# Performance work log

Measured on AMD Instinct MI355X. Metric: run time of the kernel, lower is better.

Reference implementation:

```python
import jax, jax.numpy as jnp
import numpy as np

N, E = 100000, 800000
H, C = 4, 32
HC = H * C


def setup_inputs() -> dict:
    key = jax.random.key(0)
    ks = jax.random.split(key, 32)

    def lin(k, fi, fo):
        return jax.random.normal(k, (fi, fo), jnp.float32) / np.sqrt(fi)

    inp = {
        "x": jax.random.normal(ks[0], (N, 2), jnp.float32),
        "edge_index": jax.random.randint(ks[1], (2, E), 0, N, jnp.int64),
        "edge_attr": jax.random.normal(ks[2], (E, 1), jnp.float32),
        # layer 0 (in=2)
        "Wq0": lin(ks[3], 2, HC), "bq0": jnp.zeros((HC,), jnp.float32),
        "Wk0": lin(ks[4], 2, HC), "bk0": jnp.zeros((HC,), jnp.float32),
        "Wv0": lin(ks[5], 2, HC), "bv0": jnp.zeros((HC,), jnp.float32),
        "We0": lin(ks[6], 1, HC),
        "Ws0": lin(ks[7], 2, HC), "bs0": jnp.zeros((HC,), jnp.float32),
        # layer 1 (in=HC)
        "Wq1": lin(ks[8], HC, HC), "bq1": jnp.zeros((HC,), jnp.float32),
        "Wk1": lin(ks[9], HC, HC), "bk1": jnp.zeros((HC,), jnp.float32),
        "Wv1": lin(ks[10], HC, HC), "bv1": jnp.zeros((HC,), jnp.float32),
        "We1": lin(ks[11], 1, HC),
        "Ws1": lin(ks[12], HC, HC), "bs1": jnp.zeros((HC,), jnp.float32),
        # classifier
        "Wc1": lin(ks[13], HC, 128), "bc1": jnp.zeros((128,), jnp.float32),
        "Wc2": lin(ks[14], 128, 64), "bc2": jnp.zeros((64,), jnp.float32),
        "Wc3": lin(ks[15], 64, 1), "bc3": jnp.zeros((1,), jnp.float32),
    }
    return inp


def _tconv(x, src, dst, edge_attr, Wq, bq, Wk, bk, Wv, bv, We, Ws, bs):
    # PyG TransformerConv (concat=True, root_weight=True, beta=False)
    n = x.shape[0]
    q = (x @ Wq + bq).reshape(n, H, C)
    k = (x @ Wk + bk).reshape(n, H, C)
    v = (x @ Wv + bv).reshape(n, H, C)
    e = (edge_attr @ We).reshape(-1, H, C)            # [E,H,C]
    k_j = k[src] + e
    v_j = v[src] + e
    alpha = jnp.einsum("ehc,ehc->eh", q[dst], k_j) / np.sqrt(C)  # [E,H]
    m = jax.ops.segment_max(alpha, dst, num_segments=n)          # [n,H]
    m = jnp.where(jnp.isfinite(m), m, 0.0)            # nodes with no in-edges
    ex = jnp.exp(alpha - m[dst])
    denom = jax.ops.segment_sum(ex, dst, num_segments=n)
    w = ex / (denom[dst] + 1e-16)                      # per-edge softmax weight
    out = jax.ops.segment_sum(v_j * w[:, :, None], dst, num_segments=n)
    return out.reshape(n, HC) + x @ Ws + bs


def reference(x, edge_index, edge_attr,
              Wq0, bq0, Wk0, bk0, Wv0, bv0, We0, Ws0, bs0,
              Wq1, bq1, Wk1, bk1, Wv1, bv1, We1, Ws1, bs1,
              Wc1, bc1, Wc2, bc2, Wc3, bc3):
    src, dst = edge_index[0], edge_index[1]
    h = jax.nn.relu(_tconv(x, src, dst, edge_attr, Wq0, bq0, Wk0, bk0, Wv0, bv0, We0, Ws0, bs0))
    h = jax.nn.relu(_tconv(h, src, dst, edge_attr, Wq1, bq1, Wk1, bk1, Wv1, bv1, We1, Ws1, bs1))
    # classifier (dropout inactive in eval)
    h = jax.nn.relu(h @ Wc1 + bc1)
    h = jax.nn.relu(h @ Wc2 + bc2)
    return h @ Wc3 + bc3
```

## Files before the change

kernel.cpp:

```cpp
#include <hip/hip_runtime.h>
#include <hip/hip_bf16.h>
#include <cstdio>
#include <cstdint>


typedef short s16x8 __attribute__((ext_vector_type(8)));
typedef float f32x4 __attribute__((ext_vector_type(4)));

static inline int cdiv(int a, int b) { return (a + b - 1) / b; }

#define EXP2F(x) __builtin_amdgcn_exp2f(x)
#define LOG2E 1.4426950408889634f
#define RSC 0.17677669529663687f

__device__ __forceinline__ float bflo(unsigned u) {
    union { unsigned i; float f; } x; x.i = u << 16; return x.f;
}
__device__ __forceinline__ float bfhi(unsigned u) {
    union { unsigned i; float f; } x; x.i = u & 0xffff0000u; return x.f;
}
__device__ __forceinline__ unsigned short f2b(float f) {
    __hip_bfloat16 h = __float2bfloat16(f);
    return *reinterpret_cast<unsigned short*>(&h);
}
__device__ __forceinline__ unsigned packbf(float lo, float hi) {
    return (unsigned)f2b(lo) | ((unsigned)f2b(hi) << 16);
}


__global__ __launch_bounds__(256) void hist_kernel(const int* __restrict__ dst, int E,
                                                   int* __restrict__ counts) {
    int e = blockIdx.x * 256 + threadIdx.x;
    if (e < E) atomicAdd(&counts[dst[e]], 1);
}

__global__ __launch_bounds__(256) void scan_sums(const int* __restrict__ counts, int n,
                                                 int* __restrict__ bsums) {
    __shared__ int red[256];
    int base = blockIdx.x * 2048 + threadIdx.x * 8;
    int s = 0;
#pragma unroll
    for (int j = 0; j < 8; ++j) {
        int i = base + j;
        if (i < n) s += counts[i];
    }
    red[threadIdx.x] = s;
    __syncthreads();
    for (int off = 128; off > 0; off >>= 1) {
        if (threadIdx.x < off) red[threadIdx.x] += red[threadIdx.x + off];
        __syncthreads();
    }
    if (threadIdx.x == 0) bsums[blockIdx.x] = red[0];
}

__global__ void scan_mid(int* bsums, int nb, int* offsets, int n) {
    if (blockIdx.x == 0 && threadIdx.x == 0) {
        int run = 0;
        for (int i = 0; i < nb; ++i) { int t = bsums[i]; bsums[i] = run; run += t; }
        offsets[n] = run;
    }
}

__global__ __launch_bounds__(256) void scan_out(const int* __restrict__ counts, int n,
                                                const int* __restrict__ bsums,
                                                int* __restrict__ offsets) {
    __shared__ int tsum[256];
    int base = blockIdx.x * 2048 + threadIdx.x * 8;
    int v[8];
    int s = 0;
#pragma unroll
    for (int j = 0; j < 8; ++j) {
        int i = base + j;
        v[j] = (i < n) ? counts[i] : 0;
        s += v[j];
    }
    tsum[threadIdx.x] = s;
    __syncthreads();
    for (int off = 1; off < 256; off <<= 1) {
        int x = (threadIdx.x >= (unsigned)off) ? tsum[threadIdx.x - off] : 0;
        __syncthreads();
        tsum[threadIdx.x] += x;
        __syncthreads();
    }
    int excl = tsum[threadIdx.x] - s + bsums[blockIdx.x];
#pragma unroll
    for (int j = 0; j < 8; ++j) {
        int i = base + j;
        if (i < n) { offsets[i] = excl; excl += v[j]; }
    }
}

__global__ __launch_bounds__(256) void scatter_kernel(const int* __restrict__ src,
                                                      const int* __restrict__ dst,
                                                      const float* __restrict__ ea, int E,
                                                      const int* __restrict__ offsets,
                                                      int* __restrict__ counts,
                                                      int2* __restrict__ csr) {
    int e = blockIdx.x * 256 + threadIdx.x;
    if (e >= E) return;
    int d = dst[e];
    int r = atomicSub(&counts[d], 1);
    int p = offsets[d] + r - 1;
    csr[p] = make_int2(src[e] << 9, __float_as_int(ea[e]));
}


__global__ __launch_bounds__(256) void pack_w_kernel(
    const float* __restrict__ Wq1, const float* __restrict__ Wk1,
    const float* __restrict__ Wv1, const float* __restrict__ Ws1,
    const float* __restrict__ Wc1, const float* __restrict__ Wc2,
    unsigned short* __restrict__ wpk,
    const float* __restrict__ Wq0, const float* __restrict__ bq0,
    const float* __restrict__ Wk0, const float* __restrict__ bk0,
    const float* __restrict__ We0, float* __restrict__ gcoef) {
    if (blockIdx.x == 352) {
        int t = threadIdx.x;
        if (t < 48) {
            int h = t / 12, r = t % 12, i = r >> 2, j = r & 3;
            const float* A = (i == 0) ? Wq0 : (i == 1) ? (Wq0 + 128) : bq0;
            const float* B = (j == 0) ? Wk0 : (j == 1) ? (Wk0 + 128) : (j == 2) ? We0 : bk0;
            float s = 0.f;
            for (int c = 0; c < 32; ++c) s += A[h * 32 + c] * B[h * 32 + c];
            gcoef[h * 12 + i * 4 + j] = s * (RSC * LOG2E);
        }
        return;
    }
    int idx = blockIdx.x * 256 + threadIdx.x;
    int local, COLS;
    const float* W;
    if (idx < 81920) {
        int m = idx >> 14;
        local = idx & 16383;
        COLS = 128;
        W = (m == 0) ? Wq1 : (m == 1) ? Wk1 : (m == 2) ? Wv1 : (m == 3) ? Ws1 : Wc1;
    } else {
        local = idx - 81920;
        COLS = 64;
        W = Wc2;
    }
    int CT = COLS >> 4;
    int j = local & 7, lane = (local >> 3) & 63, t = local >> 9;
    int ct = t % CT, kc = t / CT;
    int k = kc * 32 + ((lane >> 4) << 3) + j;
    int nn = (ct << 4) + (lane & 15);
    wpk[idx] = f2b(W[k * COLS + nn]);
}


__global__ __launch_bounds__(256) void agg0_kernel(
    const float* __restrict__ x, const float* __restrict__ gcoef,
    float4* __restrict__ agg4,
    const int* __restrict__ offsets, const int2* __restrict__ csr, int n_nodes) {
    int tid = blockIdx.x * 256 + threadIdx.x;
    int n = tid >> 2, h = tid & 3;
    if (n >= n_nodes) return;
    float2 xn = ((const float2*)x)[n];
    const float4* G4 = (const float4*)gcoef;
    float4 g0 = G4[h * 3 + 0], g1 = G4[h * 3 + 1], g2 = G4[h * 3 + 2];
    float c0 = fmaf(xn.y, g1.x, fmaf(xn.x, g0.x, g2.x));
    float c1 = fmaf(xn.y, g1.y, fmaf(xn.x, g0.y, g2.y));
    float c2 = fmaf(xn.y, g1.z, fmaf(xn.x, g0.z, g2.z));
    float c3 = fmaf(xn.y, g1.w, fmaf(xn.x, g0.w, g2.w));
    int beg = offsets[n], end = offsets[n + 1];
    float d = 0.f, X0 = 0.f, X1 = 0.f, EA = 0.f;
    for (int j = beg; j < end; ++j) {
        int2 ce = csr[j];
        float e = __int_as_float(ce.y);
        float2 xs = *(const float2*)((const char*)x + (((unsigned)ce.x) >> 6));
        float al = fmaf(c0, xs.x, fmaf(c1, xs.y, fmaf(c2, e, c3)));
        float w = EXP2F(fminf(al, 72.f));
        d += w;
        X0 = fmaf(w, xs.x, X0);
        X1 = fmaf(w, xs.y, X1);
        EA = fmaf(w, e, EA);
    }
    agg4[(size_t)n * 4 + h] = make_float4(X0, X1, EA, d);
}


__global__ __launch_bounds__(256) void expand0_kernel(
    const float* __restrict__ x, const float4* __restrict__ agg4,
    const float* __restrict__ Wv, const float* __restrict__ bv,
    const float* __restrict__ We, const float* __restrict__ Ws,
    const float* __restrict__ bs, uint2* __restrict__ H0, int n_nodes) {
    int gid = blockIdx.x * 256 + threadIdx.x;
    int n = gid >> 5, g = gid & 31;
    if (n >= n_nodes) return;
    int h = g >> 3;
    float4 ag = agg4[(size_t)n * 4 + h];
    float inv = 1.f / (ag.w + 1e-16f);
    float2 xn = ((const float2*)x)[n];
    float4 wv0 = ((const float4*)Wv)[g], wv1 = ((const float4*)(Wv + 128))[g];
    float4 we = ((const float4*)We)[g], bv4 = ((const float4*)bv)[g];
    float4 ws0 = ((const float4*)Ws)[g], ws1 = ((const float4*)(Ws + 128))[g];
    float4 bs4 = ((const float4*)bs)[g];
    float o0 = fmaf(wv0.x, ag.x, fmaf(wv1.x, ag.y, fmaf(we.x, ag.z, bv4.x * ag.w))) * inv
             + fmaf(xn.x, ws0.x, fmaf(xn.y, ws1.x, bs4.x));
    float o1 = fmaf(wv0.y, ag.x, fmaf(wv1.y, ag.y, fmaf(we.y, ag.z, bv4.y * ag.w))) * inv
             + fmaf(xn.x, ws0.y, fmaf(xn.y, ws1.y, bs4.y));
    float o2 = fmaf(wv0.z, ag.x, fmaf(wv1.z, ag.y, fmaf(we.z, ag.z, bv4.z * ag.w))) * inv
             + fmaf(xn.x, ws0.z, fmaf(xn.y, ws1.z, bs4.z));
    float o3 = fmaf(wv0.w, ag.x, fmaf(wv1.w, ag.y, fmaf(we.w, ag.z, bv4.w * ag.w))) * inv
             + fmaf(xn.x, ws0.w, fmaf(xn.y, ws1.w, bs4.w));
    uint2 o;
    o.x = packbf(fmaxf(o0, 0.f), fmaxf(o1, 0.f));
    o.y = packbf(fmaxf(o2, 0.f), fmaxf(o3, 0.f));
    H0[(size_t)n * 32 + g] = o;
}


__global__ __launch_bounds__(64) void agg1_kernel(
    const uint4* __restrict__ Q4, const unsigned short* __restrict__ KV,
    const float* __restrict__ We, const uint4* __restrict__ S4,
    uint4* __restrict__ Hout, const int* __restrict__ offsets,
    const int2* __restrict__ csr, int n_nodes) {
    int lane = threadIdx.x & 63;
    int h = lane & 15, g = lane >> 4;
    int n = blockIdx.x;
    if (n >= n_nodes) return;
    size_t rb = (size_t)n * 16;
    const float sc = RSC * LOG2E;
    uint4 qp = Q4[rb + h];
    float q0 = bflo(qp.x) * sc, q1 = bfhi(qp.x) * sc;
    float q2 = bflo(qp.y) * sc, q3 = bfhi(qp.y) * sc;
    float q4 = bflo(qp.z) * sc, q5 = bfhi(qp.z) * sc;
    float q6 = bflo(qp.w) * sc, q7 = bfhi(qp.w) * sc;
    float4 wea = ((const float4*)We)[2 * h], web = ((const float4*)We)[2 * h + 1];
    float qwe = fmaf(q7, web.w, fmaf(q6, web.z, fmaf(q5, web.y, fmaf(q4, web.x,
                fmaf(q3, wea.w, fmaf(q2, wea.z, fmaf(q1, wea.y, q0 * wea.x)))))));
    qwe += __shfl_xor(qwe, 1);
    qwe += __shfl_xor(qwe, 2);
    int beg = __builtin_amdgcn_readfirstlane(offsets[n]);
    int end = __builtin_amdgcn_readfirstlane(offsets[n + 1]);
    float dA = 0.f, eA = 0.f, dB = 0.f, eB = 0.f;
    float aA0 = 0.f, aA1 = 0.f, aA2 = 0.f, aA3 = 0.f;
    float aA4 = 0.f, aA5 = 0.f, aA6 = 0.f, aA7 = 0.f;
    float aB0 = 0.f, aB1 = 0.f, aB2 = 0.f, aB3 = 0.f;
    float aB4 = 0.f, aB5 = 0.f, aB6 = 0.f, aB7 = 0.f;
    int hb = h << 4;
    for (int t = beg; t < end; t += 8) {
        int jA = t + g, jB = jA + 4;
        bool vA = jA < end, vB = jB < end;
        int2 ceA = csr[vA ? jA : beg];
        int2 ceB = csr[vB ? jB : beg];
        float eaA = __int_as_float(ceA.y), eaB = __int_as_float(ceB.y);
        const char* kvA = (const char*)KV + (size_t)(unsigned)ceA.x + hb;
        const char* kvB = (const char*)KV + (size_t)(unsigned)ceB.x + hb;
        uint4 kA = *(const uint4*)kvA;
        uint4 vA4 = *(const uint4*)(kvA + 256);
        uint4 kB = *(const uint4*)kvB;
        uint4 vB4 = *(const uint4*)(kvB + 256);
        {
            float p = fmaf(q7, bfhi(kA.w), fmaf(q6, bflo(kA.w), fmaf(q5, bfhi(kA.z),
                      fmaf(q4, bflo(kA.z), fmaf(q3, bfhi(kA.y), fmaf(q2, bflo(kA.y),
                      fmaf(q1, bfhi(kA.x), q0 * bflo(kA.x))))))));
            p += __shfl_xor(p, 1);
            p += __shfl_xor(p, 2);
            float al = fminf(fmaf(eaA, qwe, p), 72.f);
            al = vA ? al : -3.0e38f;
            float w = EXP2F(al);
            dA += w;
            eA = fmaf(w, eaA, eA);
            aA0 = fmaf(w, bflo(vA4.x), aA0); aA1 = fmaf(w, bfhi(vA4.x), aA1);
            aA2 = fmaf(w, bflo(vA4.y), aA2); aA3 = fmaf(w, bfhi(vA4.y), aA3);
            aA4 = fmaf(w, bflo(vA4.z), aA4); aA5 = fmaf(w, bfhi(vA4.z), aA5);
            aA6 = fmaf(w, bflo(vA4.w), aA6); aA7 = fmaf(w, bfhi(vA4.w), aA7);
        }
        {
            float p = fmaf(q7, bfhi(kB.w), fmaf(q6, bflo(kB.w), fmaf(q5, bfhi(kB.z),
                      fmaf(q4, bflo(kB.z), fmaf(q3, bfhi(kB.y), fmaf(q2, bflo(kB.y),
                      fmaf(q1, bfhi(kB.x), q0 * bflo(kB.x))))))));
            p += __shfl_xor(p, 1);
            p += __shfl_xor(p, 2);
            float al = fminf(fmaf(eaB, qwe, p), 72.f);
            al = vB ? al : -3.0e38f;
            float w = EXP2F(al);
            dB += w;
            eB = fmaf(w, eaB, eB);
            aB0 = fmaf(w, bflo(vB4.x), aB0); aB1 = fmaf(w, bfhi(vB4.x), aB1);
            aB2 = fmaf(w, bflo(vB4.y), aB2); aB3 = fmaf(w, bfhi(vB4.y), aB3);
            aB4 = fmaf(w, bflo(vB4.z), aB4); aB5 = fmaf(w, bfhi(vB4.z), aB5);
            aB6 = fmaf(w, bflo(vB4.w), aB6); aB7 = fmaf(w, bfhi(vB4.w), aB7);
        }
    }
    float d = dA + dB, ea = eA + eB;
    float a0 = aA0 + aB0, a1 = aA1 + aB1, a2 = aA2 + aB2, a3 = aA3 + aB3;
    float a4 = aA4 + aB4, a5 = aA5 + aB5, a6 = aA6 + aB6, a7 = aA7 + aB7;
#pragma unroll
    for (int mk = 16; mk < 64; mk <<= 1) {
        d += __shfl_xor(d, mk);
        ea += __shfl_xor(ea, mk);
        a0 += __shfl_xor(a0, mk); a1 += __shfl_xor(a1, mk);
        a2 += __shfl_xor(a2, mk); a3 += __shfl_xor(a3, mk);
        a4 += __shfl_xor(a4, mk); a5 += __shfl_xor(a5, mk);
        a6 += __shfl_xor(a6, mk); a7 += __shfl_xor(a7, mk);
    }
    if (g == 0) {
        float inv = 1.f / (d + 1e-16f);
        uint4 sp = S4[rb + h];
        float o0 = fmaf(fmaf(wea.x, ea, a0), inv, bflo(sp.x));
        float o1 = fmaf(fmaf(wea.y, ea, a1), inv, bfhi(sp.x));
        float o2 = fmaf(fmaf(wea.z, ea, a2), inv, bflo(sp.y));
        float o3 = fmaf(fmaf(wea.w, ea, a3), inv, bfhi(sp.y));
        float o4 = fmaf(fmaf(web.x, ea, a4), inv, bflo(sp.z));
        float o5 = fmaf(fmaf(web.y, ea, a5), inv, bfhi(sp.z));
        float o6 = fmaf(fmaf(web.z, ea, a6), inv, bflo(sp.w));
        float o7 = fmaf(fmaf(web.w, ea, a7), inv, bfhi(sp.w));
        uint4 o;
        o.x = packbf(fmaxf(o0, 0.f), fmaxf(o1, 0.f));
        o.y = packbf(fmaxf(o2, 0.f), fmaxf(o3, 0.f));
        o.z = packbf(fmaxf(o4, 0.f), fmaxf(o5, 0.f));
        o.w = packbf(fmaxf(o6, 0.f), fmaxf(o7, 0.f));
        Hout[rb + h] = o;
    }
}


__global__ __launch_bounds__(256, 2) void gemm4_kernel(
    const unsigned short* __restrict__ Hb, int n_nodes,
    const unsigned short* __restrict__ wpk,
    const float* __restrict__ B0, unsigned short* __restrict__ O0, int ld0,
    const float* __restrict__ B1, unsigned short* __restrict__ O1, int ld1,
    const float* __restrict__ B2, unsigned short* __restrict__ O2, int ld2,
    const float* __restrict__ B3, unsigned short* __restrict__ O3, int ld3) {
    __shared__ __align__(16) unsigned short wbuf[16384];
    __shared__ __align__(16) char tbuf[128 * 272];
    int tid = threadIdx.x;
    int wid = tid >> 6, lane = tid & 63;
    int lr = lane & 15, lk = lane >> 4;
    int nblk = blockIdx.x * 128;

    s16x8 b[2][4];
#pragma unroll
    for (int nt = 0; nt < 2; ++nt) {
        int row = min(nblk + wid * 32 + nt * 16 + lr, n_nodes - 1);
        const s16x8* hp = (const s16x8*)(Hb + (size_t)row * 128);
#pragma unroll
        for (int kc = 0; kc < 4; ++kc) b[nt][kc] = hp[kc * 4 + lk];
    }
    const float* Bm[4] = {B0, B1, B2, B3};
    unsigned short* Om[4] = {O0, O1, O2, O3};
    int ldm[4] = {ld0, ld1, ld2, ld3};

#pragma unroll
    for (int i = 0; i < 8; ++i) {
        int c = i * 256 + tid;
        ((uint4*)wbuf)[c] = ((const uint4*)wpk)[c];
    }
#pragma unroll
    for (int mm = 0; mm < 4; ++mm) {
        __syncthreads();
        f32x4 acc[2][8];
#pragma unroll
        for (int nt = 0; nt < 2; ++nt)
#pragma unroll
            for (int ct = 0; ct < 8; ++ct) acc[nt][ct] = (f32x4){0.f, 0.f, 0.f, 0.f};
#pragma unroll
        for (int kc = 0; kc < 4; ++kc) {
#pragma unroll
            for (int ct = 0; ct < 8; ++ct) {
                s16x8 a = ((const s16x8*)wbuf)[(kc * 8 + ct) * 64 + lane];
                acc[0][ct] = __builtin_amdgcn_mfma_f32_16x16x32_bf16(a, b[0][kc], acc[0][ct], 0, 0, 0);
                acc[1][ct] = __builtin_amdgcn_mfma_f32_16x16x32_bf16(a, b[1][kc], acc[1][ct], 0, 0, 0);
            }
        }
        const float* Bp = Bm[mm];
#pragma unroll
        for (int ct = 0; ct < 8; ++ct) {
            float4 bb = *(const float4*)(Bp + ct * 16 + lk * 4);
#pragma unroll
            for (int nt = 0; nt < 2; ++nt) {
                int rnode = wid * 32 + nt * 16 + lr;
                uint2 o;
                o.x = packbf(acc[nt][ct][0] + bb.x, acc[nt][ct][1] + bb.y);
                o.y = packbf(acc[nt][ct][2] + bb.z, acc[nt][ct][3] + bb.w);
                *(uint2*)(tbuf + rnode * 272 + ct * 32 + lk * 8) = o;
            }
        }
        __syncthreads();
        unsigned short* Op = Om[mm];
        int ld = ldm[mm];
#pragma unroll
        for (int i = 0; i < 8; ++i) {
            int chunk = i * 256 + tid;
            int nd = chunk >> 4, c16 = chunk & 15;
            int ng = nblk + nd;
            uint4 v = *(const uint4*)(tbuf + nd * 272 + c16 * 16);
            if (ng < n_nodes) *(uint4*)(Op + (size_t)ng * ld + c16 * 8) = v;
        }
        if (mm < 3) {
            const uint4* ws = (const uint4*)(wpk + (mm + 1) * 16384);
#pragma unroll
            for (int i = 0; i < 8; ++i) {
                int c = i * 256 + tid;
                ((uint4*)wbuf)[c] = ws[c];
            }
        }
    }
}


__global__ __launch_bounds__(256, 2) void classifier_kernel(
    const unsigned short* __restrict__ H1b, int n_nodes,
    const unsigned short* __restrict__ wc1p, const float* __restrict__ bc1,
    const unsigned short* __restrict__ wc2p, const float* __restrict__ bc2,
    const float* __restrict__ Wc3, const float* __restrict__ bc3,
    float* __restrict__ out) {
    __shared__ __align__(16) unsigned short w1s[16384];
    __shared__ __align__(16) unsigned short w2s[8192];
    __shared__ __align__(16) char lds_raw[4 * 16 * 272];
    int tid = threadIdx.x;
    int wid = tid >> 6, lane = tid & 63;
    int lr = lane & 15, lk = lane >> 4;
    int nb = blockIdx.x * 64 + wid * 16;
    char* tile = lds_raw + wid * 16 * 272;

#pragma unroll
    for (int i = 0; i < 8; ++i)
        ((uint4*)w1s)[i * 256 + tid] = ((const uint4*)wc1p)[i * 256 + tid];
#pragma unroll
    for (int i = 0; i < 4; ++i)
        ((uint4*)w2s)[i * 256 + tid] = ((const uint4*)wc2p)[i * 256 + tid];

    s16x8 b[4];
    {
        int row = min(nb + lr, n_nodes - 1);
        const s16x8* hp = (const s16x8*)(H1b + (size_t)row * 128);
#pragma unroll
        for (int kc = 0; kc < 4; ++kc) b[kc] = hp[kc * 4 + lk];
    }
    __syncthreads();
    f32x4 acc[8];
#pragma unroll
    for (int ct = 0; ct < 8; ++ct) acc[ct] = (f32x4){0.f, 0.f, 0.f, 0.f};
#pragma unroll
    for (int kc = 0; kc < 4; ++kc)
#pragma unroll
        for (int ct = 0; ct < 8; ++ct) {
            s16x8 a = ((const s16x8*)w1s)[(kc * 8 + ct) * 64 + lane];
            acc[ct] = __builtin_amdgcn_mfma_f32_16x16x32_bf16(a, b[kc], acc[ct], 0, 0, 0);
        }
#pragma unroll
    for (int ct = 0; ct < 8; ++ct) {
        float4 bb = *(const float4*)(bc1 + ct * 16 + lk * 4);
        uint2 o;
        o.x = packbf(fmaxf(acc[ct][0] + bb.x, 0.f), fmaxf(acc[ct][1] + bb.y, 0.f));
        o.y = packbf(fmaxf(acc[ct][2] + bb.z, 0.f), fmaxf(acc[ct][3] + bb.w, 0.f));
        *(uint2*)(tile + lr * 272 + ct * 32 + lk * 8) = o;
    }
    __syncthreads();
    s16x8 b2[4];
#pragma unroll
    for (int kc = 0; kc < 4; ++kc)
        b2[kc] = *(const s16x8*)(tile + lr * 272 + kc * 64 + lk * 16);
    f32x4 acc2[4];
#pragma unroll
    for (int ct = 0; ct < 4; ++ct) acc2[ct] = (f32x4){0.f, 0.f, 0.f, 0.f};
#pragma unroll
    for (int kc = 0; kc < 4; ++kc)
#pragma unroll
        for (int ct = 0; ct < 4; ++ct) {
            s16x8 a = ((const s16x8*)w2s)[(kc * 4 + ct) * 64 + lane];
            acc2[ct] = __builtin_amdgcn_mfma_f32_16x16x32_bf16(a, b2[kc], acc2[ct], 0, 0, 0);
        }
    float part = 0.f;
#pragma unroll
    for (int ct = 0; ct < 4; ++ct) {
        int ch0 = ct * 16 + lk * 4;
        float4 bb = *(const float4*)(bc2 + ch0);
        float4 w3 = *(const float4*)(Wc3 + ch0);
        part += fmaxf(acc2[ct][0] + bb.x, 0.f) * w3.x;
        part += fmaxf(acc2[ct][1] + bb.y, 0.f) * w3.y;
        part += fmaxf(acc2[ct][2] + bb.z, 0.f) * w3.z;
        part += fmaxf(acc2[ct][3] + bb.w, 0.f) * w3.w;
    }
    part += __shfl_xor(part, 16);
    part += __shfl_xor(part, 32);
    if (lk == 0) {
        int node = nb + lr;
        if (node < n_nodes) out[node] = part + bc3[0];
    }
}


extern "C" void kernel_launch(void* const* d_in, const int* in_sizes, int n_in,
                              void* d_out, int out_size, void* d_ws, size_t ws_size,
                              hipStream_t stream) {
    const float* x = (const float*)d_in[0];
    const int* ei = (const int*)d_in[1];
    const float* ea = (const float*)d_in[2];
    const float *Wq0 = (const float*)d_in[3], *bq0 = (const float*)d_in[4];
    const float *Wk0 = (const float*)d_in[5], *bk0 = (const float*)d_in[6];
    const float *Wv0 = (const float*)d_in[7], *bv0 = (const float*)d_in[8];
    const float* We0 = (const float*)d_in[9];
    const float *Ws0 = (const float*)d_in[10], *bs0 = (const float*)d_in[11];
    const float *Wq1 = (const float*)d_in[12], *bq1 = (const float*)d_in[13];
    const float *Wk1 = (const float*)d_in[14], *bk1 = (const float*)d_in[15];
    const float *Wv1 = (const float*)d_in[16], *bv1 = (const float*)d_in[17];
    const float* We1 = (const float*)d_in[18];
    const float *Ws1 = (const float*)d_in[19], *bs1 = (const float*)d_in[20];
    const float *Wc1 = (const float*)d_in[21], *bc1 = (const float*)d_in[22];
    const float *Wc2 = (const float*)d_in[23], *bc2 = (const float*)d_in[24];
    const float *Wc3 = (const float*)d_in[25], *bc3 = (const float*)d_in[26];

    const int N = in_sizes[0] / 2;
    const int E = in_sizes[2];
    const int* src = ei;
    const int* dst = ei + E;

    size_t NM = (size_t)N * 128;
    float4* agg4 = (float4*)d_ws;
    float* gcoef = (float*)(agg4 + (size_t)N * 4);
    unsigned short* H0b = (unsigned short*)(gcoef + 64);
    unsigned short* Qb = H0b + NM;
    unsigned short* KV = Qb + NM;
    unsigned short* S1b = KV + 2 * NM;
    unsigned short* wpk = S1b + NM;
    int* counts = (int*)(wpk + 90112);
    int* offsets = counts + N;
    int* bsums = offsets + N + 1;
    int2* csr = (int2*)(bsums + 256);
    size_t need = (size_t)((char*)(csr + E) - (char*)d_ws);
    if (need > ws_size) {
        fprintf(stderr, "kernel_launch: ws too small (need %zu, have %zu)\n", need, ws_size);
        return;
    }

    const int NB_SCAN = cdiv(N, 2048);

    hipMemsetAsync(counts, 0, (size_t)N * 4, stream);
    hist_kernel<<<cdiv(E, 256), 256, 0, stream>>>(dst, E, counts);
    scan_sums<<<NB_SCAN, 256, 0, stream>>>(counts, N, bsums);
    scan_mid<<<1, 64, 0, stream>>>(bsums, NB_SCAN, offsets, N);
    scan_out<<<NB_SCAN, 256, 0, stream>>>(counts, N, bsums, offsets);
    scatter_kernel<<<cdiv(E, 256), 256, 0, stream>>>(src, dst, ea, E, offsets, counts, csr);
    pack_w_kernel<<<353, 256, 0, stream>>>(Wq1, Wk1, Wv1, Ws1, Wc1, Wc2, wpk,
                                           Wq0, bq0, Wk0, bk0, We0, gcoef);

    agg0_kernel<<<cdiv(N * 4, 256), 256, 0, stream>>>(
        x, gcoef, agg4, offsets, csr, N);
    expand0_kernel<<<cdiv(N * 32, 256), 256, 0, stream>>>(
        x, agg4, Wv0, bv0, We0, Ws0, bs0, (uint2*)H0b, N);

    gemm4_kernel<<<cdiv(N, 128), 256, 0, stream>>>(
        H0b, N, wpk,
        bq1, Qb, 128,
        bk1, KV, 256,
        bv1, KV + 128, 256,
        bs1, S1b, 128);
    agg1_kernel<<<N, 64, 0, stream>>>(
        (const uint4*)Qb, KV, We1, (const uint4*)S1b, (uint4*)S1b,
        offsets, csr, N);

    classifier_kernel<<<cdiv(N, 64), 256, 0, stream>>>(
        S1b, N, wpk + 65536, bc1, wpk + 81920, bc2, Wc3, bc3, (float*)d_out);
}
```

Before: 360.3 us.

## Fuse hist with weight packing, agg0 with expand0, and pack agg1 four waves per block

Merges the edge histogram and weight-packing kernels into one launch and fuses the layer-0 aggregation with its expansion through shared memory. This removes the agg4 intermediate buffer round trip and two kernel launches. agg1 now runs four nodes per 256-thread block instead of one node per 64-thread block, which cuts block scheduling overhead. The fused agg0x_kernel adds a block-wide barrier that can stall on high-degree nodes.

```diff
diff --git a/kernel.cpp b/kernel.cpp
--- a/kernel.cpp
+++ b/kernel.cpp
@@ -28,11 +28,55 @@
 }
 
 
-__global__ __launch_bounds__(256) void hist_kernel(const int* __restrict__ dst, int E,
-                                                   int* __restrict__ counts) {
-    int e = blockIdx.x * 256 + threadIdx.x;
-    if (e < E) atomicAdd(&counts[dst[e]], 1);
-}
+__global__ __launch_bounds__(256) void histpack_kernel(
+    const int* __restrict__ dst, int E, int* __restrict__ counts, int nb_hist,
+    const float* __restrict__ Wq1, const float* __restrict__ Wk1,
+    const float* __restrict__ Wv1, const float* __restrict__ Ws1,
+    const float* __restrict__ Wc1, const float* __restrict__ Wc2,
+    unsigned short* __restrict__ wpk,
+    const float* __restrict__ Wq0, const float* __restrict__ bq0,
+    const float* __restrict__ Wk0, const float* __restrict__ bk0,
+    const float* __restrict__ We0, float* __restrict__ gcoef) {
+    int bid = blockIdx.x;
+    if (bid < nb_hist) {
+        int e = bid * 256 + threadIdx.x;
+        if (e < E) atomicAdd(&counts[dst[e]], 1);
+        return;
+    }
+    int pb = bid - nb_hist;
+    if (pb == 352) {
+        int t = threadIdx.x;
+        if (t < 48) {
+            int h = t / 12, r = t % 12, i = r >> 2, j = r & 3;
+            const float* A = (i == 0) ? Wq0 : (i == 1) ? (Wq0 + 128) : bq0;
+            const float* B = (j == 0) ? Wk0 : (j == 1) ? (Wk0 + 128) : (j == 2) ? We0 : bk0;
+            float s = 0.f;
+            for (int c = 0; c < 32; ++c) s += A[h * 32 + c] * B[h * 32 + c];
+            gcoef[h * 12 + i * 4 + j] = s * (RSC * LOG2E);
+        }
+        return;
+    }
+    int idx = pb * 256 + threadIdx.x;
+    int local, COLS;
+    const float* W;
+    if (idx < 81920) {
+        int m = idx >> 14;
+        local = idx & 16383;
+        COLS = 128;
+        W = (m == 0) ? Wq1 : (m == 1) ? Wk1 : (m == 2) ? Wv1 : (m == 3) ? Ws1 : Wc1;
+    } else {
+        local = idx - 81920;
+        COLS = 64;
+        W = Wc2;
+    }
+    int CT = COLS >> 4;
+    int j = local & 7, lane = (local >> 3) & 63, t = local >> 9;
+    int ct = t % CT, kc = t / CT;
+    int k = kc * 32 + ((lane >> 4) << 3) + j;
+    int nn = (ct << 4) + (lane & 15);
+    wpk[idx] = f2b(W[k * COLS + nn]);
+}
+
 
 __global__ __launch_bounds__(256) void scan_sums(const int* __restrict__ counts, int n,
                                                  int* __restrict__ bsums) {
@@ -105,118 +149,80 @@
 }
 
 
-__global__ __launch_bounds__(256) void pack_w_kernel(
-    const float* __restrict__ Wq1, const float* __restrict__ Wk1,
-    const float* __restrict__ Wv1, const float* __restrict__ Ws1,
-    const float* __restrict__ Wc1, const float* __restrict__ Wc2,
-    unsigned short* __restrict__ wpk,
-    const float* __restrict__ Wq0, const float* __restrict__ bq0,
-    const float* __restrict__ Wk0, const float* __restrict__ bk0,
-    const float* __restrict__ We0, float* __restrict__ gcoef) {
-    if (blockIdx.x == 352) {
-        int t = threadIdx.x;
-        if (t < 48) {
-            int h = t / 12, r = t % 12, i = r >> 2, j = r & 3;
-            const float* A = (i == 0) ? Wq0 : (i == 1) ? (Wq0 + 128) : bq0;
-            const float* B = (j == 0) ? Wk0 : (j == 1) ? (Wk0 + 128) : (j == 2) ? We0 : bk0;
-            float s = 0.f;
-            for (int c = 0; c < 32; ++c) s += A[h * 32 + c] * B[h * 32 + c];
-            gcoef[h * 12 + i * 4 + j] = s * (RSC * LOG2E);
-        }
-        return;
-    }
-    int idx = blockIdx.x * 256 + threadIdx.x;
-    int local, COLS;
-    const float* W;
-    if (idx < 81920) {
-        int m = idx >> 14;
-        local = idx & 16383;
-        COLS = 128;
-        W = (m == 0) ? Wq1 : (m == 1) ? Wk1 : (m == 2) ? Wv1 : (m == 3) ? Ws1 : Wc1;
-    } else {
-        local = idx - 81920;
-        COLS = 64;
-        W = Wc2;
-    }
-    int CT = COLS >> 4;
-    int j = local & 7, lane = (local >> 3) & 63, t = local >> 9;
-    int ct = t % CT, kc = t / CT;
-    int k = kc * 32 + ((lane >> 4) << 3) + j;
-    int nn = (ct << 4) + (lane & 15);
-    wpk[idx] = f2b(W[k * COLS + nn]);
-}
-
-
-__global__ __launch_bounds__(256) void agg0_kernel(
+__global__ __launch_bounds__(256) void agg0x_kernel(
     const float* __restrict__ x, const float* __restrict__ gcoef,
-    float4* __restrict__ agg4,
-    const int* __restrict__ offsets, const int2* __restrict__ csr, int n_nodes) {
-    int tid = blockIdx.x * 256 + threadIdx.x;
-    int n = tid >> 2, h = tid & 3;
-    if (n >= n_nodes) return;
-    float2 xn = ((const float2*)x)[n];
-    const float4* G4 = (const float4*)gcoef;
-    float4 g0 = G4[h * 3 + 0], g1 = G4[h * 3 + 1], g2 = G4[h * 3 + 2];
-    float c0 = fmaf(xn.y, g1.x, fmaf(xn.x, g0.x, g2.x));
-    float c1 = fmaf(xn.y, g1.y, fmaf(xn.x, g0.y, g2.y));
-    float c2 = fmaf(xn.y, g1.z, fmaf(xn.x, g0.z, g2.z));
-    float c3 = fmaf(xn.y, g1.w, fmaf(xn.x, g0.w, g2.w));
-    int beg = offsets[n], end = offsets[n + 1];
-    float d = 0.f, X0 = 0.f, X1 = 0.f, EA = 0.f;
-    for (int j = beg; j < end; ++j) {
-        int2 ce = csr[j];
-        float e = __int_as_float(ce.y);
-        float2 xs = *(const float2*)((const char*)x + (((unsigned)ce.x) >> 6));
-        float al = fmaf(c0, xs.x, fmaf(c1, xs.y, fmaf(c2, e, c3)));
-        float w = EXP2F(fminf(al, 72.f));
-        d += w;
-        X0 = fmaf(w, xs.x, X0);
-        X1 = fmaf(w, xs.y, X1);
-        EA = fmaf(w, e, EA);
-    }
-    agg4[(size_t)n * 4 + h] = make_float4(X0, X1, EA, d);
-}
-
-
-__global__ __launch_bounds__(256) void expand0_kernel(
-    const float* __restrict__ x, const float4* __restrict__ agg4,
     const float* __restrict__ Wv, const float* __restrict__ bv,
     const float* __restrict__ We, const float* __restrict__ Ws,
-    const float* __restrict__ bs, uint2* __restrict__ H0, int n_nodes) {
-    int gid = blockIdx.x * 256 + threadIdx.x;
-    int n = gid >> 5, g = gid & 31;
-    if (n >= n_nodes) return;
-    int h = g >> 3;
-    float4 ag = agg4[(size_t)n * 4 + h];
-    float inv = 1.f / (ag.w + 1e-16f);
-    float2 xn = ((const float2*)x)[n];
+    const float* __restrict__ bs, uint2* __restrict__ H0,
+    const int* __restrict__ offsets, const int2* __restrict__ csr, int n_nodes) {
+    __shared__ float4 sm[256];
+    int t = threadIdx.x;
+    int nb = blockIdx.x * 64;
+    {
+        int n = nb + (t >> 2), h = t & 3;
+        if (n < n_nodes) {
+            float2 xn = ((const float2*)x)[n];
+            const float4* G4 = (const float4*)gcoef;
+            float4 g0 = G4[h * 3 + 0], g1 = G4[h * 3 + 1], g2 = G4[h * 3 + 2];
+            float c0 = fmaf(xn.y, g1.x, fmaf(xn.x, g0.x, g2.x));
+            float c1 = fmaf(xn.y, g1.y, fmaf(xn.x, g0.y, g2.y));
+            float c2 = fmaf(xn.y, g1.z, fmaf(xn.x, g0.z, g2.z));
+            float c3 = fmaf(xn.y, g1.w, fmaf(xn.x, g0.w, g2.w));
+            int beg = offsets[n], end = offsets[n + 1];
+            float d = 0.f, X0 = 0.f, X1 = 0.f, EA = 0.f;
+            for (int j = beg; j < end; ++j) {
+                int2 ce = csr[j];
+                float e = __int_as_float(ce.y);
+                float2 xs = *(const float2*)((const char*)x + (((unsigned)ce.x) >> 6));
+                float al = fmaf(c0, xs.x, fmaf(c1, xs.y, fmaf(c2, e, c3)));
+                float w = EXP2F(fminf(al, 72.f));
+                d += w;
+                X0 = fmaf(w, xs.x, X0);
+                X1 = fmaf(w, xs.y, X1);
+                EA = fmaf(w, e, EA);
+            }
+            sm[t] = make_float4(X0, X1, EA, d);
+        }
+    }
+    __syncthreads();
+    int g = t & 31;
     float4 wv0 = ((const float4*)Wv)[g], wv1 = ((const float4*)(Wv + 128))[g];
     float4 we = ((const float4*)We)[g], bv4 = ((const float4*)bv)[g];
     float4 ws0 = ((const float4*)Ws)[g], ws1 = ((const float4*)(Ws + 128))[g];
     float4 bs4 = ((const float4*)bs)[g];
-    float o0 = fmaf(wv0.x, ag.x, fmaf(wv1.x, ag.y, fmaf(we.x, ag.z, bv4.x * ag.w))) * inv
-             + fmaf(xn.x, ws0.x, fmaf(xn.y, ws1.x, bs4.x));
-    float o1 = fmaf(wv0.y, ag.x, fmaf(wv1.y, ag.y, fmaf(we.y, ag.z, bv4.y * ag.w))) * inv
-             + fmaf(xn.x, ws0.y, fmaf(xn.y, ws1.y, bs4.y));
-    float o2 = fmaf(wv0.z, ag.x, fmaf(wv1.z, ag.y, fmaf(we.z, ag.z, bv4.z * ag.w))) * inv
-             + fmaf(xn.x, ws0.z, fmaf(xn.y, ws1.z, bs4.z));
-    float o3 = fmaf(wv0.w, ag.x, fmaf(wv1.w, ag.y, fmaf(we.w, ag.z, bv4.w * ag.w))) * inv
-             + fmaf(xn.x, ws0.w, fmaf(xn.y, ws1.w, bs4.w));
-    uint2 o;
-    o.x = packbf(fmaxf(o0, 0.f), fmaxf(o1, 0.f));
-    o.y = packbf(fmaxf(o2, 0.f), fmaxf(o3, 0.f));
-    H0[(size_t)n * 32 + g] = o;
-}
-
-
-__global__ __launch_bounds__(64) void agg1_kernel(
+    int h = g >> 3;
+#pragma unroll
+    for (int it = 0; it < 8; ++it) {
+        int ln = it * 8 + (t >> 5);
+        int n2 = nb + ln;
+        if (n2 >= n_nodes) break;
+        float4 ag = sm[ln * 4 + h];
+        float inv = 1.f / (ag.w + 1e-16f);
+        float2 xn = ((const float2*)x)[n2];
+        float o0 = fmaf(wv0.x, ag.x, fmaf(wv1.x, ag.y, fmaf(we.x, ag.z, bv4.x * ag.w))) * inv
+                 + fmaf(xn.x, ws0.x, fmaf(xn.y, ws1.x, bs4.x));
+        float o1 = fmaf(wv0.y, ag.x, fmaf(wv1.y, ag.y, fmaf(we.y, ag.z, bv4.y * ag.w))) * inv
+                 + fmaf(xn.x, ws0.y, fmaf(xn.y, ws1.y, bs4.y));
+        float o2 = fmaf(wv0.z, ag.x, fmaf(wv1.z, ag.y, fmaf(we.z, ag.z, bv4.z * ag.w))) * inv
+                 + fmaf(xn.x, ws0.z, fmaf(xn.y, ws1.z, bs4.z));
+        float o3 = fmaf(wv0.w, ag.x, fmaf(wv1.w, ag.y, fmaf(we.w, ag.z, bv4.w * ag.w))) * inv
+                 + fmaf(xn.x, ws0.w, fmaf(xn.y, ws1.w, bs4.w));
+        uint2 o;
+        o.x = packbf(fmaxf(o0, 0.f), fmaxf(o1, 0.f));
+        o.y = packbf(fmaxf(o2, 0.f), fmaxf(o3, 0.f));
+        H0[(size_t)n2 * 32 + g] = o;
+    }
+}
+
+
+__global__ __launch_bounds__(256) void agg1_kernel(
     const uint4* __restrict__ Q4, const unsigned short* __restrict__ KV,
     const float* __restrict__ We, const uint4* __restrict__ S4,
     uint4* __restrict__ Hout, const int* __restrict__ offsets,
     const int2* __restrict__ csr, int n_nodes) {
-    int lane = threadIdx.x & 63;
+    int wid = threadIdx.x >> 6, lane = threadIdx.x & 63;
     int h = lane & 15, g = lane >> 4;
-    int n = blockIdx.x;
+    int n = blockIdx.x * 4 + wid;
     if (n >= n_nodes) return;
     size_t rb = (size_t)n * 16;
     const float sc = RSC * LOG2E;
@@ -509,8 +515,7 @@
     const int* dst = ei + E;
 
     size_t NM = (size_t)N * 128;
-    float4* agg4 = (float4*)d_ws;
-    float* gcoef = (float*)(agg4 + (size_t)N * 4);
+    float* gcoef = (float*)d_ws;
     unsigned short* H0b = (unsigned short*)(gcoef + 64);
     unsigned short* Qb = H0b + NM;
     unsigned short* KV = Qb + NM;
@@ -518,29 +523,28 @@
     unsigned short* wpk = S1b + NM;
     int* counts = (int*)(wpk + 90112);
     int* offsets = counts + N;
-    int* bsums = offsets + N + 1;
-    int2* csr = (int2*)(bsums + 256);
+    int* bsums = offsets + N + 2;
+    int2* csr = (int2*)(bsums + 64);
     size_t need = (size_t)((char*)(csr + E) - (char*)d_ws);
     if (need > ws_size) {
         fprintf(stderr, "kernel_launch: ws too small (need %zu, have %zu)\n", need, ws_size);
         return;
     }
 
+    const int NB_HIST = cdiv(E, 256);
     const int NB_SCAN = cdiv(N, 2048);
 
     hipMemsetAsync(counts, 0, (size_t)N * 4, stream);
-    hist_kernel<<<cdiv(E, 256), 256, 0, stream>>>(dst, E, counts);
+    histpack_kernel<<<NB_HIST + 353, 256, 0, stream>>>(
+        dst, E, counts, NB_HIST, Wq1, Wk1, Wv1, Ws1, Wc1, Wc2, wpk,
+        Wq0, bq0, Wk0, bk0, We0, gcoef);
     scan_sums<<<NB_SCAN, 256, 0, stream>>>(counts, N, bsums);
     scan_mid<<<1, 64, 0, stream>>>(bsums, NB_SCAN, offsets, N);
     scan_out<<<NB_SCAN, 256, 0, stream>>>(counts, N, bsums, offsets);
-    scatter_kernel<<<cdiv(E, 256), 256, 0, stream>>>(src, dst, ea, E, offsets, counts, csr);
-    pack_w_kernel<<<353, 256, 0, stream>>>(Wq1, Wk1, Wv1, Ws1, Wc1, Wc2, wpk,
-                                           Wq0, bq0, Wk0, bk0, We0, gcoef);
-
-    agg0_kernel<<<cdiv(N * 4, 256), 256, 0, stream>>>(
-        x, gcoef, agg4, offsets, csr, N);
-    expand0_kernel<<<cdiv(N * 32, 256), 256, 0, stream>>>(
-        x, agg4, Wv0, bv0, We0, Ws0, bs0, (uint2*)H0b, N);
+    scatter_kernel<<<NB_HIST, 256, 0, stream>>>(src, dst, ea, E, offsets, counts, csr);
+
+    agg0x_kernel<<<cdiv(N, 64), 256, 0, stream>>>(
+        x, gcoef, Wv0, bv0, We0, Ws0, bs0, (uint2*)H0b, offsets, csr, N);
 
     gemm4_kernel<<<cdiv(N, 128), 256, 0, stream>>>(
         H0b, N, wpk,
@@ -548,7 +552,7 @@
         bk1, KV, 256,
         bv1, KV + 128, 256,
         bs1, S1b, 128);
-    agg1_kernel<<<N, 64, 0, stream>>>(
+    agg1_kernel<<<cdiv(N, 4), 256, 0, stream>>>(
         (const uint4*)Qb, KV, We1, (const uint4*)S1b, (uint4*)S1b,
         offsets, csr, N);
 
```

New measurement: 348.1 us. 1.04x faster.
